# Performance work log

Hardware: AMD Instinct MI355X
Metric: run time of the kernel (lower is better)

## Reference

```python
import jax, jax.numpy as jnp
import numpy as np

N = 50000          # num nodes
E = 800000         # num edges
H, C = 2, 64       # heads, per-head channels (hidden_dim=64)
IN_DIM = 128
EDGE_DIM = 32
NEG_SLOPE = 0.2


def setup_inputs() -> dict:
    key = jax.random.key(0)
    ks = jax.random.split(key, 20)
    s = 0.05
    inp = {
        'x': jax.random.normal(ks[0], (N, IN_DIM), jnp.float32),
        'edge_index': jax.random.randint(ks[1], (2, E), 0, N, jnp.int64),
        'edge_attr': jax.random.normal(ks[2], (E, EDGE_DIM), jnp.float32),
    }
    k = 3
    for l in range(3):
        inp[f'Wl{l}'] = jax.random.normal(ks[k], (IN_DIM, H * C), jnp.float32) * s; k += 1
        inp[f'Wr{l}'] = jax.random.normal(ks[k], (IN_DIM, H * C), jnp.float32) * s; k += 1
        inp[f'We{l}'] = jax.random.normal(ks[k], (EDGE_DIM, H * C), jnp.float32) * s; k += 1
        inp[f'att{l}'] = jax.random.normal(ks[k], (H, C), jnp.float32) * s; k += 1
        inp[f'b{l}'] = jnp.zeros((H * C,), jnp.float32)
    return inp


def gatv2_layer(x, src, dst, edge_attr, Wl, Wr, We, att, b):
    # PyG GATv2Conv (concat=True, share_weights=False):
    #   e_ij = att . LeakyReLU(Wl x_j + Wr x_i + We edge_ij)
    #   alpha = softmax_j over neighborhood of dst i; out_i = sum_j alpha_ij * (Wl x_j)
    xl = (x @ Wl).reshape(-1, H, C)              # [N,H,C] source transform
    xr = (x @ Wr).reshape(-1, H, C)              # [N,H,C] target transform
    ea = (edge_attr @ We).reshape(-1, H, C)      # [E,H,C]
    xj = xl[src]                                 # [E,H,C] gather source
    e = jax.nn.leaky_relu(xj + xr[dst] + ea, NEG_SLOPE)
    logits = jnp.einsum('ehc,hc->eh', e, att)    # [E,H]
    # segment softmax over dst neighborhoods
    m = jax.ops.segment_max(logits, dst, num_segments=N)  # [N,H]
    m = jnp.where(jnp.isfinite(m), m, 0.0)
    ex = jnp.exp(logits - m[dst])
    denom = jax.ops.segment_sum(ex, dst, num_segments=N)  # [N,H]
    alpha = ex / (denom[dst] + 1e-16)            # [E,H]
    out = jax.ops.segment_sum(alpha[:, :, None] * xj, dst, num_segments=N)  # [N,H,C]
    return out.reshape(-1, H * C) + b


def reference(x, edge_index, edge_attr,
              Wl0, Wr0, We0, att0, b0,
              Wl1, Wr1, We1, att1, b1,
              Wl2, Wr2, We2, att2, b2):
    src, dst = edge_index[0], edge_index[1]
    h = gatv2_layer(x, src, dst, edge_attr, Wl0, Wr0, We0, att0, b0)
    h = jax.nn.relu(h)
    h = gatv2_layer(h, src, dst, edge_attr, Wl1, Wr1, We1, att1, b1)
    h = jax.nn.relu(h)
    h = gatv2_layer(h, src, dst, edge_attr, Wl2, Wr2, We2, att2, b2)
    return h
```

## Files before the change

### kernel.cpp

```cpp
#include <hip/hip_runtime.h>

typedef unsigned int u32;
typedef unsigned short u16;
typedef __attribute__((ext_vector_type(8))) short bf16x8;
typedef __attribute__((ext_vector_type(4))) float f32x4;

__device__ __forceinline__ u16 f2b(float f){
  u32 x = __float_as_uint(f);
  u32 r = (x + 0x7fffu + ((x >> 16) & 1u)) >> 16;
  return (u16)r;
}
__device__ __forceinline__ float b2f(u16 h){ return __uint_as_float((u32)h << 16); }
__device__ __forceinline__ float bl(u32 u){ return __uint_as_float(u << 16); }
__device__ __forceinline__ float bh(u32 u){ return __uint_as_float(u & 0xffff0000u); }


__global__ void k_detect(const u32* __restrict__ ei, int n, u32* __restrict__ flag){
  int t = blockIdx.x * blockDim.x + threadIdx.x;
  u32 v = 0;
  if (t < n) v = ei[2 * t + 1];
  unsigned long long b = __ballot(v != 0u);
  if ((threadIdx.x & 63) == 0 && b) atomicOr(flag, 1u);
}

__global__ void k_convhist(const int* __restrict__ ei, int* __restrict__ src, int* __restrict__ dst,
                           int* __restrict__ deg, int E, const u32* __restrict__ flag){
  int e = blockIdx.x * blockDim.x + threadIdx.x;
  if (e >= E) return;
  bool is64 = (*flag == 0u);
  int s, d;
  if (is64){ s = ei[2 * e]; d = ei[2 * (E + e)]; }
  else     { s = ei[e];     d = ei[E + e]; }
  src[e] = s; dst[e] = d;
  atomicAdd(&deg[d], 1);
}

__global__ __launch_bounds__(1024) void k_scan(const int* __restrict__ deg, int* __restrict__ seg, int n){
  __shared__ int wsum[16];
  __shared__ int carry_s;
  int t = threadIdx.x, lane = t & 63, w = t >> 6;
  if (t == 0) carry_s = 0;
  __syncthreads();
  int n4 = (n + 3) >> 2;
  for (int base = 0; base < n4; base += 1024){
    int g = base + t;
    int i0 = g * 4;
    int4 v = make_int4(0, 0, 0, 0);
    if (g < n4){
      if (i0 + 3 < n) v = *(const int4*)(deg + i0);
      else {
        if (i0 < n)     v.x = deg[i0];
        if (i0 + 1 < n) v.y = deg[i0 + 1];
        if (i0 + 2 < n) v.z = deg[i0 + 2];
      }
    }
    int tot = v.x + v.y + v.z + v.w;
    int x = tot;
    #pragma unroll
    for (int off = 1; off < 64; off <<= 1){
      int y = __shfl_up(x, off);
      if (lane >= off) x += y;
    }
    if (lane == 63) wsum[w] = x;
    __syncthreads();
    if (w == 0 && lane < 16){
      int sv = wsum[lane];
      #pragma unroll
      for (int off = 1; off < 16; off <<= 1){
        int y = __shfl_up(sv, off);
        if (lane >= off) sv += y;
      }
      wsum[lane] = sv;
    }
    __syncthreads();
    int woff = (w > 0) ? wsum[w - 1] : 0;
    int carry = carry_s;
    int incl = carry + woff + x;
    int excl = incl - tot;
    if (i0 < n){
      seg[i0] = excl;
      if (i0 + 1 < n) seg[i0 + 1] = excl + v.x;
      if (i0 + 2 < n) seg[i0 + 2] = excl + v.x + v.y;
      if (i0 + 3 < n) seg[i0 + 3] = excl + v.x + v.y + v.z;
    }
    __syncthreads();
    if (t == 1023) carry_s = incl;
    __syncthreads();
  }
  if (threadIdx.x == 0) seg[n] = carry_s;
}

__global__ void k_scatter(const int* __restrict__ src, const int* __restrict__ dst,
                          const int* __restrict__ seg, int* __restrict__ cur,
                          int* __restrict__ ssrc, int* __restrict__ sdst,
                          int* __restrict__ seid, int E){
  int e = blockIdx.x * blockDim.x + threadIdx.x;
  if (e >= E) return;
  int d = dst[e];
  int pos = seg[d] + atomicAdd(&cur[d], 1);
  ssrc[pos] = src[e];
  sdst[pos] = d;
  seid[pos] = e;
}

__global__ void k_sorte(const int* __restrict__ seid, const float* __restrict__ eattr,
                        u16* __restrict__ ea2, int E){
  int e = blockIdx.x * blockDim.x + threadIdx.x;
  if (e >= E) return;
  const float4* srow = (const float4*)(eattr + (size_t)seid[e] * 32);
  u32 pk[16];
  #pragma unroll
  for (int i = 0; i < 8; i++){
    float4 v = srow[i];
    pk[2*i]   = (u32)f2b(v.x) | ((u32)f2b(v.y) << 16);
    pk[2*i+1] = (u32)f2b(v.z) | ((u32)f2b(v.w) << 16);
  }
  uint4* drow = (uint4*)(ea2 + (size_t)e * 32);
  drow[0] = make_uint4(pk[0], pk[1], pk[2], pk[3]);
  drow[1] = make_uint4(pk[4], pk[5], pk[6], pk[7]);
  drow[2] = make_uint4(pk[8], pk[9], pk[10], pk[11]);
  drow[3] = make_uint4(pk[12], pk[13], pk[14], pk[15]);
}

__global__ __launch_bounds__(256) void k_prepw(
    const float* __restrict__ W0, const float* __restrict__ W1, const float* __restrict__ W2,
    const float* __restrict__ W3, const float* __restrict__ W4, const float* __restrict__ W5,
    u16* __restrict__ WtH, u16* __restrict__ WtL)
{
  int mat = blockIdx.z;
  const float* W = (mat == 0) ? W0 : (mat == 1) ? W1 : (mat == 2) ? W2 :
                   (mat == 3) ? W3 : (mat == 4) ? W4 : W5;
  __shared__ float tile[32][33];
  int kt = blockIdx.x * 32, ct = blockIdx.y * 32;
  int tr = threadIdx.x & 31, ti = threadIdx.x >> 5;
  #pragma unroll
  for (int j = 0; j < 4; j++){
    int kk = ti + 8 * j;
    tile[kk][tr] = W[(size_t)(kt + kk) * 128 + ct + tr];
  }
  __syncthreads();
  #pragma unroll
  for (int j = 0; j < 4; j++){
    int cc = ti + 8 * j;
    float v = tile[tr][cc];
    u16 hi = f2b(v);
    u16 lo = f2b(v - b2f(hi));
    size_t o = (size_t)mat * 16384 + (size_t)(ct + cc) * 128 + kt + tr;
    WtH[o] = hi;
    WtL[o] = lo;
  }
}

__global__ __launch_bounds__(256) void k_gemm2(
    const float* __restrict__ A,
    const u16* __restrict__ WtH, const u16* __restrict__ WtL,
    u16* __restrict__ xlb, u16* __restrict__ xrb, int nrows)
{
  __shared__ u16 sAH[64][72], sAL[64][72];
  __shared__ u16 sWH[128][72], sWL[128][72];
  int t = threadIdx.x, wv = t >> 6, lane = t & 63;
  int col = lane & 15, kg = lane >> 4;
  int r0 = blockIdx.x * 64;
  int mat = blockIdx.y;
  const u16* WHb = WtH + (size_t)mat * 16384;
  const u16* WLb = WtL + (size_t)mat * 16384;

  f32x4 acc[4][2];
  #pragma unroll
  for (int m = 0; m < 4; m++)
    #pragma unroll
    for (int n = 0; n < 2; n++)
      acc[m][n] = (f32x4){0.f, 0.f, 0.f, 0.f};

  int ar = t >> 2, ak = (t & 3) << 4;
  int wc = t >> 1, wk = (t & 1) << 5;

  for (int kh = 0; kh < 2; kh++){
    __syncthreads();
    {
      int gr = r0 + ar;
      const float* ap = A + (size_t)gr * 128 + kh * 64 + ak;
      float4 va = {0,0,0,0}, vb = {0,0,0,0}, vc = {0,0,0,0}, vd = {0,0,0,0};
      if (gr < nrows){
        va = *(const float4*)ap; vb = *(const float4*)(ap + 4);
        vc = *(const float4*)(ap + 8); vd = *(const float4*)(ap + 12);
      }
      float fv[16] = { va.x, va.y, va.z, va.w, vb.x, vb.y, vb.z, vb.w,
                       vc.x, vc.y, vc.z, vc.w, vd.x, vd.y, vd.z, vd.w };
      u32 hp[8], lp[8];
      #pragma unroll
      for (int i = 0; i < 8; i++){
        u16 h0 = f2b(fv[2*i]),   h1 = f2b(fv[2*i+1]);
        u16 l0 = f2b(fv[2*i]   - b2f(h0));
        u16 l1 = f2b(fv[2*i+1] - b2f(h1));
        hp[i] = (u32)h0 | ((u32)h1 << 16);
        lp[i] = (u32)l0 | ((u32)l1 << 16);
      }
      *(uint4*)&sAH[ar][ak]     = make_uint4(hp[0], hp[1], hp[2], hp[3]);
      *(uint4*)&sAH[ar][ak + 8] = make_uint4(hp[4], hp[5], hp[6], hp[7]);
      *(uint4*)&sAL[ar][ak]     = make_uint4(lp[0], lp[1], lp[2], lp[3]);
      *(uint4*)&sAL[ar][ak + 8] = make_uint4(lp[4], lp[5], lp[6], lp[7]);
    }
    {
      const u16* gh = WHb + (size_t)wc * 128 + kh * 64 + wk;
      const u16* gl = WLb + (size_t)wc * 128 + kh * 64 + wk;
      uint4 h0 = *(const uint4*)gh, h1 = *(const uint4*)(gh + 8);
      uint4 h2 = *(const uint4*)(gh + 16), h3 = *(const uint4*)(gh + 24);
      uint4 l0 = *(const uint4*)gl, l1 = *(const uint4*)(gl + 8);
      uint4 l2 = *(const uint4*)(gl + 16), l3 = *(const uint4*)(gl + 24);
      *(uint4*)&sWH[wc][wk]      = h0; *(uint4*)&sWH[wc][wk + 8]  = h1;
      *(uint4*)&sWH[wc][wk + 16] = h2; *(uint4*)&sWH[wc][wk + 24] = h3;
      *(uint4*)&sWL[wc][wk]      = l0; *(uint4*)&sWL[wc][wk + 8]  = l1;
      *(uint4*)&sWL[wc][wk + 16] = l2; *(uint4*)&sWL[wc][wk + 24] = l3;
    }
    __syncthreads();
    #pragma unroll
    for (int ks = 0; ks < 2; ks++){
      bf16x8 bhi0 = *(const bf16x8*)&sWH[wv*32 + col]     [ks*32 + kg*8];
      bf16x8 bhi1 = *(const bf16x8*)&sWH[wv*32 + 16 + col][ks*32 + kg*8];
      bf16x8 blo0 = *(const bf16x8*)&sWL[wv*32 + col]     [ks*32 + kg*8];
      bf16x8 blo1 = *(const bf16x8*)&sWL[wv*32 + 16 + col][ks*32 + kg*8];
      #pragma unroll
      for (int m = 0; m < 4; m++){
        bf16x8 ahv = *(const bf16x8*)&sAH[m*16 + col][ks*32 + kg*8];
        bf16x8 alv = *(const bf16x8*)&sAL[m*16 + col][ks*32 + kg*8];
        acc[m][0] = __builtin_amdgcn_mfma_f32_16x16x32_bf16(ahv, bhi0, acc[m][0], 0, 0, 0);
        acc[m][0] = __builtin_amdgcn_mfma_f32_16x16x32_bf16(alv, bhi0, acc[m][0], 0, 0, 0);
        acc[m][0] = __builtin_amdgcn_mfma_f32_16x16x32_bf16(ahv, blo0, acc[m][0], 0, 0, 0);
        acc[m][1] = __builtin_amdgcn_mfma_f32_16x16x32_bf16(ahv, bhi1, acc[m][1], 0, 0, 0);
        acc[m][1] = __builtin_amdgcn_mfma_f32_16x16x32_bf16(alv, bhi1, acc[m][1], 0, 0, 0);
        acc[m][1] = __builtin_amdgcn_mfma_f32_16x16x32_bf16(ahv, blo1, acc[m][1], 0, 0, 0);
      }
    }
  }
  u16* ob = mat ? xrb : xlb;
  #pragma unroll
  for (int m = 0; m < 4; m++){
    #pragma unroll
    for (int n = 0; n < 2; n++){
      #pragma unroll
      for (int r = 0; r < 4; r++){
        int row = r0 + m*16 + kg*4 + r;
        int c   = wv*32 + n*16 + col;
        if (row < nrows) ob[(size_t)row * 128 + c] = f2b(acc[m][n][r]);
      }
    }
  }
}

__global__ __launch_bounds__(256) void k_edge(
    const int* __restrict__ ssrc, const int* __restrict__ sdst,
    const u16* __restrict__ ea2,
    const u16* __restrict__ xlb, const u16* __restrict__ xrb,
    const float* __restrict__ We, const float* __restrict__ att,
    float2* __restrict__ pr2, int ntiles, int E)
{
  __shared__ float sD[4][16][136];
  int wv = threadIdx.x >> 6, lane = threadIdx.x & 63;
  int col = lane & 15, kg = lane >> 4;
  int er = lane >> 2, q = lane & 3;

  bf16x8 bw[8];
  #pragma unroll
  for (int c = 0; c < 8; c++)
    #pragma unroll
    for (int j = 0; j < 8; j++)
      bw[c][j] = (short)f2b(We[(kg * 8 + j) * 128 + c * 16 + col]);
  float attq[32];
  #pragma unroll
  for (int i = 0; i < 8; i++){
    float4 a4 = *(const float4*)(att + q * 32 + i * 4);
    attq[4*i] = a4.x; attq[4*i+1] = a4.y; attq[4*i+2] = a4.z; attq[4*i+3] = a4.w;
  }

  int wid0 = blockIdx.x * 4 + wv;
  int nw = gridDim.x * 4;
  for (int t = wid0; t < ntiles; t += nw){
    int e0 = t * 16;
    bf16x8 a = *(const bf16x8*)(ea2 + (size_t)(e0 + col) * 32 + kg * 8);
    #pragma unroll
    for (int c = 0; c < 8; c++){
      f32x4 d = __builtin_amdgcn_mfma_f32_16x16x32_bf16(a, bw[c], (f32x4){0.f,0.f,0.f,0.f}, 0, 0, 0);
      #pragma unroll
      for (int r = 0; r < 4; r++)
        sD[wv][kg * 4 + r][c * 16 + col] = d[r];
    }
    int p = e0 + er;
    int sn = ssrc[p], dn = sdst[p];
    const u16* xj = xlb + (size_t)sn * 128 + q * 32;
    const u16* xi = xrb + (size_t)dn * 128 + q * 32;
    uint4 jq[4], iq[4];
    jq[0] = *(const uint4*)(xj);      jq[1] = *(const uint4*)(xj + 8);
    jq[2] = *(const uint4*)(xj + 16); jq[3] = *(const uint4*)(xj + 24);
    iq[0] = *(const uint4*)(xi);      iq[1] = *(const uint4*)(xi + 8);
    iq[2] = *(const uint4*)(xi + 16); iq[3] = *(const uint4*)(xi + 24);
    const float* drow = &sD[wv][er][q * 32];

    float acc = 0.f;
    #pragma unroll
    for (int k = 0; k < 4; k++){
      float4 d0 = *(const float4*)(drow + k * 8);
      float4 d1 = *(const float4*)(drow + k * 8 + 4);
      u32 jw[4] = { jq[k].x, jq[k].y, jq[k].z, jq[k].w };
      u32 iw[4] = { iq[k].x, iq[k].y, iq[k].z, iq[k].w };
      float dv[8] = { d0.x, d0.y, d0.z, d0.w, d1.x, d1.y, d1.z, d1.w };
      #pragma unroll
      for (int m = 0; m < 4; m++){
        float v0 = dv[2*m]   + bl(jw[m]) + bl(iw[m]);
        float v1 = dv[2*m+1] + bh(jw[m]) + bh(iw[m]);
        v0 = fmaxf(v0, 0.2f * v0);
        v1 = fmaxf(v1, 0.2f * v1);
        acc = fmaf(v0, attq[k*8 + 2*m], acc);
        acc = fmaf(v1, attq[k*8 + 2*m + 1], acc);
      }
    }
    acc += __shfl_xor(acc, 1);
    float other = __shfl_xor(acc, 2);
    if (q == 0 && p < E){
      float l0 = fminf(acc, 80.f), l1 = fminf(other, 80.f);
      pr2[p] = make_float2(__expf(l0), __expf(l1));
    }
  }
}

template<int RELU>
__global__ __launch_bounds__(256) void k_seg2(
    const int* __restrict__ seg, const int* __restrict__ ssrc,
    const float2* __restrict__ pr2,
    const u16* __restrict__ xlb, const float* __restrict__ bias,
    float* __restrict__ out, int N)
{
  int wid  = blockIdx.x * 4 + (threadIdx.x >> 6);
  int lane = threadIdx.x & 63;
  if (wid >= N) return;
  int c0 = lane * 2, head = lane >> 5;

  int p0 = seg[wid], p1 = seg[wid + 1];
  float2 bv = *(const float2*)(bias + c0);
  float s = 0.f, o0 = 0.f, o1 = 0.f;

  for (int p = p0; p < p1; p += 8){
#define STAGE(K) \
    int i##K = (p + K < p1) ? (p + K) : (p1 - 1); \
    int sn##K = ssrc[i##K]; \
    float2 q##K = pr2[i##K]; \
    u32 xv##K = *(const u32*)(xlb + (size_t)sn##K * 128 + c0);
    STAGE(0) STAGE(1) STAGE(2) STAGE(3) STAGE(4) STAGE(5) STAGE(6) STAGE(7)
#undef STAGE
#define ACCUM(K) { \
    float e##K = head ? q##K.y : q##K.x; \
    if (p + K >= p1) e##K = 0.f; \
    s += e##K; \
    o0 = fmaf(e##K, bl(xv##K), o0); \
    o1 = fmaf(e##K, bh(xv##K), o1); }
    ACCUM(0) ACCUM(1) ACCUM(2) ACCUM(3) ACCUM(4) ACCUM(5) ACCUM(6) ACCUM(7)
#undef ACCUM
  }
  float inv = 1.0f / (s + 1e-16f);
  float r0 = fmaf(o0, inv, bv.x);
  float r1 = fmaf(o1, inv, bv.y);
  if (RELU){ r0 = fmaxf(r0, 0.f); r1 = fmaxf(r1, 0.f); }
  *(float2*)(out + (size_t)wid * 128 + c0) = make_float2(r0, r1);
}

extern "C" void kernel_launch(void* const* d_in, const int* in_sizes, int n_in,
                              void* d_out, int out_size, void* d_ws, size_t ws_size,
                              hipStream_t stream)
{
  const float* x     = (const float*)d_in[0];
  const int*   ei    = (const int*)  d_in[1];
  const float* eattr = (const float*)d_in[2];
  const float* Wp[3][5];
  for (int l = 0; l < 3; l++)
    for (int j = 0; j < 5; j++)
      Wp[l][j] = (const float*)d_in[3 + l * 5 + j];

  int N = in_sizes[0] / 128;
  int E = in_sizes[2] / 32;

  char* w = (char*)d_ws;
  auto alloc = [&](size_t bytes) -> char* {
    char* p = w; w += (bytes + 255) & ~(size_t)255; return p;
  };
  float* xr   = (float*)alloc((size_t)N * 128 * 4);
  u16*   xlb  = (u16*)  alloc((size_t)N * 128 * 2);
  u16*   xrb  = (u16*)  alloc((size_t)N * 128 * 2);
  u16*   ea2  = (u16*)  alloc((size_t)(E + 64) * 32 * 2);
  float2* prb = (float2*)alloc((size_t)E * 8);
  u16*   WtH  = (u16*)  alloc((size_t)6 * 16384 * 2);
  u16*   WtL  = (u16*)  alloc((size_t)6 * 16384 * 2);
  int* srcA   = (int*)alloc((size_t)E * 4);
  int* dstA   = (int*)alloc((size_t)E * 4);
  int* ssrc   = (int*)alloc((size_t)(E + 64) * 4);
  int* sdst   = (int*)alloc((size_t)(E + 64) * 4);
  int* seid   = (int*)alloc((size_t)E * 4);
  int* deg    = (int*)alloc((size_t)N * 4);
  int* cur    = (int*)alloc((size_t)N * 4);
  int* seg    = (int*)alloc((size_t)(N + 1) * 4);
  u32* flag   = (u32*)alloc(256);

  hipMemsetAsync(deg,  0, (size_t)N * 4, stream);
  hipMemsetAsync(cur,  0, (size_t)N * 4, stream);
  hipMemsetAsync(flag, 0, 4, stream);
  hipMemsetAsync(ssrc + E, 0, 64 * 4, stream);
  hipMemsetAsync(sdst + E, 0, 64 * 4, stream);

  int ndet = (E < 16384) ? E : 16384;
  k_detect<<<(ndet + 255) / 256, 256, 0, stream>>>((const u32*)ei, ndet, flag);
  int gE = (E + 255) / 256;
  k_convhist<<<gE, 256, 0, stream>>>(ei, srcA, dstA, deg, E, flag);
  k_scan<<<1, 1024, 0, stream>>>(deg, seg, N);
  k_scatter<<<gE, 256, 0, stream>>>(srcA, dstA, seg, cur, ssrc, sdst, seid, E);
  k_sorte<<<gE, 256, 0, stream>>>(seid, eattr, ea2, E);
  dim3 gp(4, 4, 6);
  k_prepw<<<gp, 256, 0, stream>>>(Wp[0][0], Wp[0][1], Wp[1][0], Wp[1][1], Wp[2][0], Wp[2][1], WtH, WtL);

  int gS = (N + 3) / 4;
  int ntiles = (E + 15) / 16;
  int gEdge = (ntiles + 3) / 4; if (gEdge > 2048) gEdge = 2048;
  dim3 gG2((N + 63) / 64, 2);

  const float* hin = x;
  for (int l = 0; l < 3; l++){
    k_gemm2<<<gG2, 256, 0, stream>>>(hin, WtH + (size_t)l * 2 * 16384, WtL + (size_t)l * 2 * 16384, xlb, xrb, N);
    k_edge<<<gEdge, 256, 0, stream>>>(ssrc, sdst, ea2, xlb, xrb, Wp[l][2], Wp[l][3], prb, ntiles, E);
    float* outp = (l == 2) ? (float*)d_out : xr;
    if (l == 2) k_seg2<0><<<gS, 256, 0, stream>>>(seg, ssrc, prb, xlb, Wp[l][4], outp, N);
    else        k_seg2<1><<<gS, 256, 0, stream>>>(seg, ssrc, prb, xlb, Wp[l][4], outp, N);
    hin = xr;
  }
}
```

Before: 537.5 us.

## Parallelize degree scan, fuse edge-attr sort into scatter, prefetch gathers in edge/seg kernels

The single-block scan is replaced by a three-kernel multi-block scan (block sums, scan of sums, per-block finalize). The edge-attribute reorder is folded into the scatter kernel, which now writes bf16 attributes straight to their sorted position and drops the seid array and a kernel. Both k_edge and k_seg2 are software-pipelined so the gathers for the next tile or chunk are issued before the current one is computed. The attention vector is also packed to bf16 to cut register use. The prefetching raises register pressure, and bf16 attention weights add a small precision loss.

```diff
diff --git a/kernel.cpp b/kernel.cpp
--- a/kernel.cpp
+++ b/kernel.cpp
@@ -35,79 +35,87 @@
   atomicAdd(&deg[d], 1);
 }
 
-__global__ __launch_bounds__(1024) void k_scan(const int* __restrict__ deg, int* __restrict__ seg, int n){
+__global__ __launch_bounds__(256) void k_scan1(const int* __restrict__ deg, int* __restrict__ bsum, int n){
+  int b = blockIdx.x, t = threadIdx.x, lane = t & 63, wv = t >> 6;
+  int i0 = b * 1024 + t * 4;
+  int4 v = make_int4(0,0,0,0);
+  if (i0 + 3 < n) v = *(const int4*)(deg + i0);
+  else { if (i0 < n) v.x = deg[i0]; if (i0+1 < n) v.y = deg[i0+1]; if (i0+2 < n) v.z = deg[i0+2]; }
+  int s = v.x + v.y + v.z + v.w;
+  #pragma unroll
+  for (int off = 1; off < 64; off <<= 1) s += __shfl_xor(s, off);
+  __shared__ int ws[4];
+  if (lane == 0) ws[wv] = s;
+  __syncthreads();
+  if (t == 0) bsum[b] = ws[0] + ws[1] + ws[2] + ws[3];
+}
+
+__global__ __launch_bounds__(1024) void k_scan2(int* __restrict__ bsum, int nb, int* __restrict__ segN){
+  int t = threadIdx.x, lane = t & 63, w = t >> 6;
+  int v = (t < nb) ? bsum[t] : 0;
+  int x = v;
+  #pragma unroll
+  for (int off = 1; off < 64; off <<= 1){
+    int y = __shfl_up(x, off);
+    if (lane >= off) x += y;
+  }
   __shared__ int wsum[16];
-  __shared__ int carry_s;
-  int t = threadIdx.x, lane = t & 63, w = t >> 6;
-  if (t == 0) carry_s = 0;
+  if (lane == 63) wsum[w] = x;
   __syncthreads();
-  int n4 = (n + 3) >> 2;
-  for (int base = 0; base < n4; base += 1024){
-    int g = base + t;
-    int i0 = g * 4;
-    int4 v = make_int4(0, 0, 0, 0);
-    if (g < n4){
-      if (i0 + 3 < n) v = *(const int4*)(deg + i0);
-      else {
-        if (i0 < n)     v.x = deg[i0];
-        if (i0 + 1 < n) v.y = deg[i0 + 1];
-        if (i0 + 2 < n) v.z = deg[i0 + 2];
-      }
-    }
-    int tot = v.x + v.y + v.z + v.w;
-    int x = tot;
-    #pragma unroll
-    for (int off = 1; off < 64; off <<= 1){
-      int y = __shfl_up(x, off);
-      if (lane >= off) x += y;
-    }
-    if (lane == 63) wsum[w] = x;
-    __syncthreads();
-    if (w == 0 && lane < 16){
-      int sv = wsum[lane];
-      #pragma unroll
-      for (int off = 1; off < 16; off <<= 1){
-        int y = __shfl_up(sv, off);
-        if (lane >= off) sv += y;
-      }
-      wsum[lane] = sv;
-    }
-    __syncthreads();
-    int woff = (w > 0) ? wsum[w - 1] : 0;
-    int carry = carry_s;
-    int incl = carry + woff + x;
-    int excl = incl - tot;
-    if (i0 < n){
-      seg[i0] = excl;
-      if (i0 + 1 < n) seg[i0 + 1] = excl + v.x;
-      if (i0 + 2 < n) seg[i0 + 2] = excl + v.x + v.y;
-      if (i0 + 3 < n) seg[i0 + 3] = excl + v.x + v.y + v.z;
-    }
-    __syncthreads();
-    if (t == 1023) carry_s = incl;
-    __syncthreads();
-  }
-  if (threadIdx.x == 0) seg[n] = carry_s;
+  if (w == 0 && lane < 16){
+    int sv = wsum[lane];
+    #pragma unroll
+    for (int off = 1; off < 16; off <<= 1){
+      int y = __shfl_up(sv, off);
+      if (lane >= off) sv += y;
+    }
+    wsum[lane] = sv;
+  }
+  __syncthreads();
+  int woff = (w > 0) ? wsum[w - 1] : 0;
+  if (t < nb) bsum[t] = woff + x - v;
+  if (t == 0) *segN = wsum[15];
+}
+
+__global__ __launch_bounds__(256) void k_scan3(const int* __restrict__ deg, const int* __restrict__ bsum,
+                                               int* __restrict__ seg, int n){
+  int b = blockIdx.x, t = threadIdx.x, lane = t & 63, wv = t >> 6;
+  int i0 = b * 1024 + t * 4;
+  int4 v = make_int4(0,0,0,0);
+  if (i0 + 3 < n) v = *(const int4*)(deg + i0);
+  else { if (i0 < n) v.x = deg[i0]; if (i0+1 < n) v.y = deg[i0+1]; if (i0+2 < n) v.z = deg[i0+2]; }
+  int s = v.x + v.y + v.z + v.w;
+  int x = s;
+  #pragma unroll
+  for (int off = 1; off < 64; off <<= 1){
+    int y = __shfl_up(x, off);
+    if (lane >= off) x += y;
+  }
+  __shared__ int ws[4];
+  if (lane == 63) ws[wv] = x;
+  __syncthreads();
+  int woff = 0;
+  #pragma unroll
+  for (int k = 0; k < 4; k++) if (k < wv) woff += ws[k];
+  int base = bsum[b] + woff + (x - s);
+  if (i0 < n)     seg[i0]     = base;
+  if (i0+1 < n)   seg[i0+1]   = base + v.x;
+  if (i0+2 < n)   seg[i0+2]   = base + v.x + v.y;
+  if (i0+3 < n)   seg[i0+3]   = base + v.x + v.y + v.z;
 }
 
 __global__ void k_scatter(const int* __restrict__ src, const int* __restrict__ dst,
                           const int* __restrict__ seg, int* __restrict__ cur,
+                          const float* __restrict__ eattr,
                           int* __restrict__ ssrc, int* __restrict__ sdst,
-                          int* __restrict__ seid, int E){
+                          u16* __restrict__ ea2, int E){
   int e = blockIdx.x * blockDim.x + threadIdx.x;
   if (e >= E) return;
   int d = dst[e];
   int pos = seg[d] + atomicAdd(&cur[d], 1);
   ssrc[pos] = src[e];
   sdst[pos] = d;
-  seid[pos] = e;
-}
-
-__global__ void k_sorte(const int* __restrict__ seid, const float* __restrict__ eattr,
-                        u16* __restrict__ ea2, int E){
-  int e = blockIdx.x * blockDim.x + threadIdx.x;
-  if (e >= E) return;
-  const float4* srow = (const float4*)(eattr + (size_t)seid[e] * 32);
+  const float4* srow = (const float4*)(eattr + (size_t)e * 32);
   u32 pk[16];
   #pragma unroll
   for (int i = 0; i < 8; i++){
@@ -115,7 +123,7 @@
     pk[2*i]   = (u32)f2b(v.x) | ((u32)f2b(v.y) << 16);
     pk[2*i+1] = (u32)f2b(v.z) | ((u32)f2b(v.w) << 16);
   }
-  uint4* drow = (uint4*)(ea2 + (size_t)e * 32);
+  uint4* drow = (uint4*)(ea2 + (size_t)pos * 32);
   drow[0] = make_uint4(pk[0], pk[1], pk[2], pk[3]);
   drow[1] = make_uint4(pk[4], pk[5], pk[6], pk[7]);
   drow[2] = make_uint4(pk[8], pk[9], pk[10], pk[11]);
@@ -266,18 +274,35 @@
     #pragma unroll
     for (int j = 0; j < 8; j++)
       bw[c][j] = (short)f2b(We[(kg * 8 + j) * 128 + c * 16 + col]);
-  float attq[32];
-  #pragma unroll
-  for (int i = 0; i < 8; i++){
-    float4 a4 = *(const float4*)(att + q * 32 + i * 4);
-    attq[4*i] = a4.x; attq[4*i+1] = a4.y; attq[4*i+2] = a4.z; attq[4*i+3] = a4.w;
-  }
-
-  int wid0 = blockIdx.x * 4 + wv;
+  u32 attp[16];
+  #pragma unroll
+  for (int i = 0; i < 16; i++)
+    attp[i] = (u32)f2b(att[q * 32 + 2*i]) | ((u32)f2b(att[q * 32 + 2*i + 1]) << 16);
+
   int nw = gridDim.x * 4;
-  for (int t = wid0; t < ntiles; t += nw){
-    int e0 = t * 16;
-    bf16x8 a = *(const bf16x8*)(ea2 + (size_t)(e0 + col) * 32 + kg * 8);
+  int t = blockIdx.x * 4 + wv;
+  if (t >= ntiles) return;
+
+  int e0 = t * 16;
+  bf16x8 a = *(const bf16x8*)(ea2 + (size_t)(e0 + col) * 32 + kg * 8);
+  int p = e0 + er;
+  int sn = ssrc[p], dn = sdst[p];
+  const u16* xjp = xlb + (size_t)sn * 128 + q * 32;
+  const u16* xip = xrb + (size_t)dn * 128 + q * 32;
+  uint4 j0 = ((const uint4*)xjp)[0], j1 = ((const uint4*)xjp)[1],
+        j2 = ((const uint4*)xjp)[2], j3 = ((const uint4*)xjp)[3];
+  uint4 i0 = ((const uint4*)xip)[0], i1 = ((const uint4*)xip)[1],
+        i2 = ((const uint4*)xip)[2], i3 = ((const uint4*)xip)[3];
+
+  while (true){
+    int t2 = t + nw;
+    bool more = (t2 < ntiles);
+    int tc = more ? t2 : t;
+    int e02 = tc * 16;
+    int p2 = e02 + er;
+    int sn2 = ssrc[p2], dn2 = sdst[p2];
+    bf16x8 a2 = *(const bf16x8*)(ea2 + (size_t)(e02 + col) * 32 + kg * 8);
+
     #pragma unroll
     for (int c = 0; c < 8; c++){
       f32x4 d = __builtin_amdgcn_mfma_f32_16x16x32_bf16(a, bw[c], (f32x4){0.f,0.f,0.f,0.f}, 0, 0, 0);
@@ -285,41 +310,43 @@
       for (int r = 0; r < 4; r++)
         sD[wv][kg * 4 + r][c * 16 + col] = d[r];
     }
-    int p = e0 + er;
-    int sn = ssrc[p], dn = sdst[p];
-    const u16* xj = xlb + (size_t)sn * 128 + q * 32;
-    const u16* xi = xrb + (size_t)dn * 128 + q * 32;
-    uint4 jq[4], iq[4];
-    jq[0] = *(const uint4*)(xj);      jq[1] = *(const uint4*)(xj + 8);
-    jq[2] = *(const uint4*)(xj + 16); jq[3] = *(const uint4*)(xj + 24);
-    iq[0] = *(const uint4*)(xi);      iq[1] = *(const uint4*)(xi + 8);
-    iq[2] = *(const uint4*)(xi + 16); iq[3] = *(const uint4*)(xi + 24);
+
+    const u16* xj2 = xlb + (size_t)sn2 * 128 + q * 32;
+    const u16* xi2 = xrb + (size_t)dn2 * 128 + q * 32;
+    uint4 nj0 = ((const uint4*)xj2)[0], nj1 = ((const uint4*)xj2)[1],
+          nj2 = ((const uint4*)xj2)[2], nj3 = ((const uint4*)xj2)[3];
+    uint4 ni0 = ((const uint4*)xi2)[0], ni1 = ((const uint4*)xi2)[1],
+          ni2 = ((const uint4*)xi2)[2], ni3 = ((const uint4*)xi2)[3];
+
     const float* drow = &sD[wv][er][q * 32];
-
     float acc = 0.f;
-    #pragma unroll
-    for (int k = 0; k < 4; k++){
-      float4 d0 = *(const float4*)(drow + k * 8);
-      float4 d1 = *(const float4*)(drow + k * 8 + 4);
-      u32 jw[4] = { jq[k].x, jq[k].y, jq[k].z, jq[k].w };
-      u32 iw[4] = { iq[k].x, iq[k].y, iq[k].z, iq[k].w };
-      float dv[8] = { d0.x, d0.y, d0.z, d0.w, d1.x, d1.y, d1.z, d1.w };
-      #pragma unroll
-      for (int m = 0; m < 4; m++){
-        float v0 = dv[2*m]   + bl(jw[m]) + bl(iw[m]);
-        float v1 = dv[2*m+1] + bh(jw[m]) + bh(iw[m]);
-        v0 = fmaxf(v0, 0.2f * v0);
-        v1 = fmaxf(v1, 0.2f * v1);
-        acc = fmaf(v0, attq[k*8 + 2*m], acc);
-        acc = fmaf(v1, attq[k*8 + 2*m + 1], acc);
-      }
-    }
+#define EPK(KO, JQ, IQ) { \
+    float4 d0 = *(const float4*)(drow + KO*8); \
+    float4 d1 = *(const float4*)(drow + KO*8 + 4); \
+    float v; u32 jw, iw, aw; \
+    jw = JQ.x; iw = IQ.x; aw = attp[KO*4+0]; \
+    v = d0.x + bl(jw) + bl(iw); v = fmaxf(v, 0.2f*v); acc = fmaf(v, bl(aw), acc); \
+    v = d0.y + bh(jw) + bh(iw); v = fmaxf(v, 0.2f*v); acc = fmaf(v, bh(aw), acc); \
+    jw = JQ.y; iw = IQ.y; aw = attp[KO*4+1]; \
+    v = d0.z + bl(jw) + bl(iw); v = fmaxf(v, 0.2f*v); acc = fmaf(v, bl(aw), acc); \
+    v = d0.w + bh(jw) + bh(iw); v = fmaxf(v, 0.2f*v); acc = fmaf(v, bh(aw), acc); \
+    jw = JQ.z; iw = IQ.z; aw = attp[KO*4+2]; \
+    v = d1.x + bl(jw) + bl(iw); v = fmaxf(v, 0.2f*v); acc = fmaf(v, bl(aw), acc); \
+    v = d1.y + bh(jw) + bh(iw); v = fmaxf(v, 0.2f*v); acc = fmaf(v, bh(aw), acc); \
+    jw = JQ.w; iw = IQ.w; aw = attp[KO*4+3]; \
+    v = d1.z + bl(jw) + bl(iw); v = fmaxf(v, 0.2f*v); acc = fmaf(v, bl(aw), acc); \
+    v = d1.w + bh(jw) + bh(iw); v = fmaxf(v, 0.2f*v); acc = fmaf(v, bh(aw), acc); }
+    EPK(0, j0, i0) EPK(1, j1, i1) EPK(2, j2, i2) EPK(3, j3, i3)
+#undef EPK
     acc += __shfl_xor(acc, 1);
     float other = __shfl_xor(acc, 2);
     if (q == 0 && p < E){
-      float l0 = fminf(acc, 80.f), l1 = fminf(other, 80.f);
-      pr2[p] = make_float2(__expf(l0), __expf(l1));
-    }
+      pr2[p] = make_float2(__expf(fminf(acc, 80.f)), __expf(fminf(other, 80.f)));
+    }
+    if (!more) break;
+    t = t2; p = p2; a = a2;
+    j0 = nj0; j1 = nj1; j2 = nj2; j3 = nj3;
+    i0 = ni0; i1 = ni1; i2 = ni2; i3 = ni3;
   }
 }
 
@@ -339,22 +366,42 @@
   float2 bv = *(const float2*)(bias + c0);
   float s = 0.f, o0 = 0.f, o1 = 0.f;
 
-  for (int p = p0; p < p1; p += 8){
-#define STAGE(K) \
-    int i##K = (p + K < p1) ? (p + K) : (p1 - 1); \
-    int sn##K = ssrc[i##K]; \
-    float2 q##K = pr2[i##K]; \
-    u32 xv##K = *(const u32*)(xlb + (size_t)sn##K * 128 + c0);
-    STAGE(0) STAGE(1) STAGE(2) STAGE(3) STAGE(4) STAGE(5) STAGE(6) STAGE(7)
-#undef STAGE
-#define ACCUM(K) { \
-    float e##K = head ? q##K.y : q##K.x; \
-    if (p + K >= p1) e##K = 0.f; \
-    s += e##K; \
-    o0 = fmaf(e##K, bl(xv##K), o0); \
-    o1 = fmaf(e##K, bh(xv##K), o1); }
-    ACCUM(0) ACCUM(1) ACCUM(2) ACCUM(3) ACCUM(4) ACCUM(5) ACCUM(6) ACCUM(7)
-#undef ACCUM
+  if (p0 < p1){
+#define LDB(K, PP, QN, XN) \
+    { int ii = (PP + K < p1) ? (PP + K) : (p1 - 1); \
+      int ss = ssrc[ii]; \
+      QN = pr2[ii]; \
+      XN = *(const u32*)(xlb + (size_t)ss * 128 + c0); }
+    float2 qa0, qa1, qa2, qa3, qa4, qa5, qa6, qa7;
+    u32 xa0, xa1, xa2, xa3, xa4, xa5, xa6, xa7;
+    LDB(0, p0, qa0, xa0) LDB(1, p0, qa1, xa1) LDB(2, p0, qa2, xa2) LDB(3, p0, qa3, xa3)
+    LDB(4, p0, qa4, xa4) LDB(5, p0, qa5, xa5) LDB(6, p0, qa6, xa6) LDB(7, p0, qa7, xa7)
+    int p = p0;
+    while (true){
+      int pn = p + 8;
+      bool more = pn < p1;
+      int pc = more ? pn : p;
+      float2 qb0, qb1, qb2, qb3, qb4, qb5, qb6, qb7;
+      u32 xb0, xb1, xb2, xb3, xb4, xb5, xb6, xb7;
+      LDB(0, pc, qb0, xb0) LDB(1, pc, qb1, xb1) LDB(2, pc, qb2, xb2) LDB(3, pc, qb3, xb3)
+      LDB(4, pc, qb4, xb4) LDB(5, pc, qb5, xb5) LDB(6, pc, qb6, xb6) LDB(7, pc, qb7, xb7)
+#define ACC(K, QN, XN) { \
+      float e = head ? QN.y : QN.x; \
+      if (p + K >= p1) e = 0.f; \
+      s += e; \
+      o0 = fmaf(e, bl(XN), o0); \
+      o1 = fmaf(e, bh(XN), o1); }
+      ACC(0, qa0, xa0) ACC(1, qa1, xa1) ACC(2, qa2, xa2) ACC(3, qa3, xa3)
+      ACC(4, qa4, xa4) ACC(5, qa5, xa5) ACC(6, qa6, xa6) ACC(7, qa7, xa7)
+#undef ACC
+      if (!more) break;
+      p = pn;
+      qa0 = qb0; xa0 = xb0; qa1 = qb1; xa1 = xb1;
+      qa2 = qb2; xa2 = xb2; qa3 = qb3; xa3 = xb3;
+      qa4 = qb4; xa4 = xb4; qa5 = qb5; xa5 = xb5;
+      qa6 = qb6; xa6 = xb6; qa7 = qb7; xa7 = xb7;
+    }
+#undef LDB
   }
   float inv = 1.0f / (s + 1e-16f);
   float r0 = fmaf(o0, inv, bv.x);
@@ -393,10 +440,10 @@
   int* dstA   = (int*)alloc((size_t)E * 4);
   int* ssrc   = (int*)alloc((size_t)(E + 64) * 4);
   int* sdst   = (int*)alloc((size_t)(E + 64) * 4);
-  int* seid   = (int*)alloc((size_t)E * 4);
   int* deg    = (int*)alloc((size_t)N * 4);
   int* cur    = (int*)alloc((size_t)N * 4);
   int* seg    = (int*)alloc((size_t)(N + 1) * 4);
+  int* bsum   = (int*)alloc(1024 * 4);
   u32* flag   = (u32*)alloc(256);
 
   hipMemsetAsync(deg,  0, (size_t)N * 4, stream);
@@ -409,9 +456,11 @@
   k_detect<<<(ndet + 255) / 256, 256, 0, stream>>>((const u32*)ei, ndet, flag);
   int gE = (E + 255) / 256;
   k_convhist<<<gE, 256, 0, stream>>>(ei, srcA, dstA, deg, E, flag);
-  k_scan<<<1, 1024, 0, stream>>>(deg, seg, N);
-  k_scatter<<<gE, 256, 0, stream>>>(srcA, dstA, seg, cur, ssrc, sdst, seid, E);
-  k_sorte<<<gE, 256, 0, stream>>>(seid, eattr, ea2, E);
+  int nb = (N + 1023) / 1024;
+  k_scan1<<<nb, 256, 0, stream>>>(deg, bsum, N);
+  k_scan2<<<1, 1024, 0, stream>>>(bsum, nb, seg + N);
+  k_scan3<<<nb, 256, 0, stream>>>(deg, bsum, seg, N);
+  k_scatter<<<gE, 256, 0, stream>>>(srcA, dstA, seg, cur, eattr, ssrc, sdst, ea2, E);
   dim3 gp(4, 4, 6);
   k_prepw<<<gp, 256, 0, stream>>>(Wp[0][0], Wp[0][1], Wp[1][0], Wp[1][1], Wp[2][0], Wp[2][1], WtH, WtL);
 
```

Result: slower. 556.9 us (+3.6%).
